# Kernel tuning notes

Hardware: AMD Instinct MI355X
Metric: run time of the kernel (lower is better)

The kernel has to match this reference:

```python
import jax, jax.numpy as jnp
import numpy as np

D = 1024
H = 16
HD = D // H
N_TEXT = 256
N_VISION = 256
N_FRAMES = 12


def setup_inputs() -> dict:
    key = jax.random.key(0)
    ks = jax.random.split(key, 10)
    s = 1.0 / np.sqrt(D)
    return {
        "text_hidden_states": jax.random.normal(ks[0], (N_TEXT, D), jnp.float32),
        "vision_hidden_states": jax.random.normal(ks[1], (N_VISION, N_FRAMES, D), jnp.float32),
        "wq": jax.random.normal(ks[2], (D, D), jnp.float32) * s,
        "bq": jnp.zeros((D,), jnp.float32),
        "wk": jax.random.normal(ks[3], (D, D), jnp.float32) * s,
        "bk": jnp.zeros((D,), jnp.float32),
        "wv": jax.random.normal(ks[4], (D, D), jnp.float32) * s,
        "bv": jnp.zeros((D,), jnp.float32),
        "wo": jax.random.normal(ks[5], (D, D), jnp.float32) * s,
        "bo": jnp.zeros((D,), jnp.float32),
    }


def reference(text_hidden_states, vision_hidden_states, wq, bq, wk, bk, wv, bv, wo, bo):
    n_text = text_hidden_states.shape[0]
    n_vision, n_frames, _ = vision_hidden_states.shape
    # projections (torch Linear: x @ W.T + b)
    q = (text_hidden_states @ wq.T + bq).reshape(n_text, H, HD)            # [t,h,d]
    k = (vision_hidden_states @ wk.T + bk).reshape(n_vision, n_frames, H, HD)  # [v,f,h,d]
    v = (vision_hidden_states @ wv.T + bv).reshape(n_vision, n_frames, H, HD)  # [v,f,h,d]
    # shared query broadcast over vision batch: scores [v,h,f,t]
    scores = jnp.einsum("vfhd,thd->vhft", k, q) / jnp.sqrt(jnp.asarray(HD, scores_dtype := q.dtype))
    probs = jax.nn.softmax(scores, axis=2)  # softmax over frames (dim=2)
    # attn_output [v,t,h,d] -> [v,t,D]
    out = jnp.einsum("vfhd,vhft->vthd", v, probs).reshape(n_vision, n_text, D)
    return out @ wo.T + bo
```

## Files before the change

### kernel.cpp

```cpp
#include <hip/hip_runtime.h>

typedef short bf16x8 __attribute__((ext_vector_type(8)));
typedef float f32x4 __attribute__((ext_vector_type(4)));

__device__ __forceinline__ unsigned short f2bf(float f) {
  union { float f; unsigned u; } x; x.f = f;
  unsigned u = x.u;
  u += 0x7fffu + ((u >> 16) & 1u);
  return (unsigned short)(u >> 16);
}

__global__ __launch_bounds__(256) void cvt_all(
    const float* __restrict__ text, const float* __restrict__ vis,
    const float* __restrict__ wq, const float* __restrict__ wk,
    const float* __restrict__ wv, const float* __restrict__ wo,
    unsigned short* __restrict__ o0, unsigned short* __restrict__ o1,
    unsigned short* __restrict__ o2, unsigned short* __restrict__ o3,
    unsigned short* __restrict__ o4, unsigned short* __restrict__ o5)
{
  long i4 = (long)blockIdx.x * 256 + threadIdx.x;
  const float* src; unsigned short* dst; long base;
  if      (i4 <   65536) { src = text; dst = o0; base = 0; }
  else if (i4 <  851968) { src = vis;  dst = o1; base = 65536; }
  else if (i4 < 1114112) { src = wq;   dst = o2; base = 851968; }
  else if (i4 < 1376256) { src = wk;   dst = o3; base = 1114112; }
  else if (i4 < 1638400) { src = wv;   dst = o4; base = 1376256; }
  else                   { src = wo;   dst = o5; base = 1638400; }
  long li = i4 - base;
  float4 f = reinterpret_cast<const float4*>(src)[li];
  uint2 u;
  u.x = (unsigned)f2bf(f.x) | ((unsigned)f2bf(f.y) << 16);
  u.y = (unsigned)f2bf(f.z) | ((unsigned)f2bf(f.w) << 16);
  reinterpret_cast<uint2*>(dst)[li] = u;
}

__global__ __launch_bounds__(256) void gemm_abt_bf16(
    const unsigned short* __restrict__ A,
    const unsigned short* __restrict__ B,
    unsigned short* __restrict__ C,
    const float* __restrict__ bias,
    int K, int lda, int ldb, int ldc)
{
  __shared__ unsigned short As[64][40];
  __shared__ unsigned short Bs[64][40];
  const int m0 = blockIdx.y * 64, n0 = blockIdx.x * 64;
  const int tid = threadIdx.x;
  const int lane = tid & 63, w = tid >> 6;
  const int wm = w >> 1, wn = w & 1;
  const int r16 = lane & 15, kg = lane >> 4;
  const int srow = tid >> 2, sseg = tid & 3;

  const f32x4 fzero = {0.f, 0.f, 0.f, 0.f};
  f32x4 acc[2][2];
#pragma unroll
  for (int i = 0; i < 2; ++i)
#pragma unroll
    for (int j = 0; j < 2; ++j) acc[i][j] = fzero;

  for (int k0 = 0; k0 < K; k0 += 32) {
    __syncthreads();
    *reinterpret_cast<int4*>(&As[srow][sseg * 8]) =
        *reinterpret_cast<const int4*>(&A[(long)(m0 + srow) * lda + k0 + sseg * 8]);
    *reinterpret_cast<int4*>(&Bs[srow][sseg * 8]) =
        *reinterpret_cast<const int4*>(&B[(long)(n0 + srow) * ldb + k0 + sseg * 8]);
    __syncthreads();
    bf16x8 a[2], b[2];
#pragma unroll
    for (int i = 0; i < 2; ++i)
      a[i] = *reinterpret_cast<const bf16x8*>(&As[wm * 32 + i * 16 + r16][kg * 8]);
#pragma unroll
    for (int j = 0; j < 2; ++j)
      b[j] = *reinterpret_cast<const bf16x8*>(&Bs[wn * 32 + j * 16 + r16][kg * 8]);
#pragma unroll
    for (int i = 0; i < 2; ++i)
#pragma unroll
      for (int j = 0; j < 2; ++j)
        acc[i][j] = __builtin_amdgcn_mfma_f32_16x16x32_bf16(a[i], b[j], acc[i][j], 0, 0, 0);
  }
#pragma unroll
  for (int i = 0; i < 2; ++i) {
#pragma unroll
    for (int j = 0; j < 2; ++j) {
      const int row = m0 + wm * 32 + i * 16 + kg * 4;
      const int col = n0 + wn * 32 + j * 16 + r16;
      const float bv = bias ? bias[col] : 0.f;
#pragma unroll
      for (int r = 0; r < 4; ++r)
        C[(long)(row + r) * ldc + col] = f2bf(acc[i][j][r] + bv);
    }
  }
}

__global__ __launch_bounds__(256) void scores_softmax(
    const unsigned short* __restrict__ Kp,
    const unsigned short* __restrict__ Qp,
    unsigned short* __restrict__ P)
{
  const int h = blockIdx.x, v = blockIdx.y;
  const int tid = threadIdx.x, lane = tid & 63, w = tid >> 6;
  const int r16 = lane & 15, kg = lane >> 4;
  __shared__ unsigned short Ks[16][72];
  __shared__ unsigned short Qs[256][72];

  if (tid < 96) {
    const int f = tid >> 3, seg = tid & 7;
    *reinterpret_cast<int4*>(&Ks[f][seg * 8]) =
        *reinterpret_cast<const int4*>(&Kp[(long)(v * 12 + f) * 1024 + h * 64 + seg * 8]);
  } else if (tid < 128) {
    const int f = 12 + ((tid - 96) >> 3), seg = (tid - 96) & 7;
    int4 z; z.x = z.y = z.z = z.w = 0;
    *reinterpret_cast<int4*>(&Ks[f][seg * 8]) = z;
  }
#pragma unroll
  for (int rep = 0; rep < 8; ++rep) {
    const int row = rep * 32 + (tid >> 3), seg = tid & 7;
    *reinterpret_cast<int4*>(&Qs[row][seg * 8]) =
        *reinterpret_cast<const int4*>(&Qp[(long)row * 1024 + h * 64 + seg * 8]);
  }
  __syncthreads();

  const f32x4 fzero = {0.f, 0.f, 0.f, 0.f};
  f32x4 acc[4];
#pragma unroll
  for (int j = 0; j < 4; ++j) acc[j] = fzero;

#pragma unroll
  for (int kk = 0; kk < 64; kk += 32) {
    bf16x8 a = *reinterpret_cast<const bf16x8*>(&Ks[r16][kk + kg * 8]);
#pragma unroll
    for (int j = 0; j < 4; ++j) {
      bf16x8 b = *reinterpret_cast<const bf16x8*>(&Qs[w * 64 + j * 16 + r16][kk + kg * 8]);
      acc[j] = __builtin_amdgcn_mfma_f32_16x16x32_bf16(a, b, acc[j], 0, 0, 0);
    }
  }
#pragma unroll
  for (int j = 0; j < 4; ++j) {
    float lm = -1e30f;
    if (kg < 3) {
#pragma unroll
      for (int r = 0; r < 4; ++r) lm = fmaxf(lm, acc[j][r] * 0.125f);
    }
    lm = fmaxf(lm, __shfl_xor(lm, 16));
    lm = fmaxf(lm, __shfl_xor(lm, 32));
    float p[4]; float ls = 0.f;
    if (kg < 3) {
#pragma unroll
      for (int r = 0; r < 4; ++r) { p[r] = __expf(acc[j][r] * 0.125f - lm); ls += p[r]; }
    }
    ls += __shfl_xor(ls, 16);
    ls += __shfl_xor(ls, 32);
    const float inv = 1.f / ls;
    if (kg < 3) {
      const int t = w * 64 + j * 16 + r16;
#pragma unroll
      for (int r = 0; r < 4; ++r)
        P[((long)v * 256 + t) * 192 + (kg * 4 + r) * 16 + h] = f2bf(p[r] * inv);
    }
  }
}

__global__ __launch_bounds__(256) void combine(
    const unsigned short* __restrict__ VPp,
    const unsigned short* __restrict__ Wo,
    const unsigned short* __restrict__ P,
    const float* __restrict__ bo,
    float* __restrict__ out)
{
  const int wgid = blockIdx.x;
  const int xcd = wgid & 7, idx = wgid >> 3;
  const int v = ((idx & 31) << 3) | xcd;
  const int n0 = (idx >> 5) << 6;

  const int tid = threadIdx.x, lane = tid & 63, w = tid >> 6;
  const int r16 = lane & 15, kg = lane >> 4;

  __shared__ unsigned short BsAll[64 * 192];
  __shared__ unsigned short VPs[2][16 * 64];
  __shared__ unsigned short Wos[2][64 * 64];

  for (int it = 0; it < 8; ++it) {
    const int hbase = it * 2;
    __syncthreads();
    {
      const int hh = tid >> 7, row = (tid >> 3) & 15, slot = tid & 7;
      int4 val;
      if (row < 12)
        val = *reinterpret_cast<const int4*>(
            &VPp[(long)(v * 12 + row) * 1024 + (hbase + hh) * 64 + slot * 8]);
      else { val.x = 0; val.y = 0; val.z = 0; val.w = 0; }
      *reinterpret_cast<int4*>(&VPs[hh][row * 64 + ((slot ^ (row & 7)) << 3)]) = val;
    }
    {
      const int hh = tid >> 7;
      const int row = (tid & 127) >> 1, slot0 = (tid & 1) * 4;
#pragma unroll
      for (int rep = 0; rep < 4; ++rep) {
        const int slot = slot0 + rep;
        *reinterpret_cast<int4*>(&Wos[hh][row * 64 + ((slot ^ (row & 7)) << 3)]) =
            *reinterpret_cast<const int4*>(
                &Wo[(long)(n0 + row) * 1024 + (hbase + hh) * 64 + slot * 8]);
      }
    }
    __syncthreads();
    const int hh = w >> 1, oh = w & 1, h = hbase + hh;
    f32x4 accp[2] = {{0.f,0.f,0.f,0.f},{0.f,0.f,0.f,0.f}};
#pragma unroll
    for (int kk = 0; kk < 64; kk += 32) {
      const int slot = (kk >> 3) + kg;
      bf16x8 a = *reinterpret_cast<const bf16x8*>(
          &VPs[hh][r16 * 64 + ((slot ^ (r16 & 7)) << 3)]);
#pragma unroll
      for (int j = 0; j < 2; ++j) {
        const int orow = oh * 32 + j * 16 + r16;
        bf16x8 b = *reinterpret_cast<const bf16x8*>(
            &Wos[hh][orow * 64 + ((slot ^ (orow & 7)) << 3)]);
        accp[j] = __builtin_amdgcn_mfma_f32_16x16x32_bf16(a, b, accp[j], 0, 0, 0);
      }
    }
#pragma unroll
    for (int j = 0; j < 2; ++j) {
#pragma unroll
      for (int r = 0; r < 4; ++r) {
        const int f = kg * 4 + r;
        if (f < 12) {
          const int o = oh * 32 + j * 16 + r16;
          const int k = f * 16 + h;
          BsAll[o * 192 + (((k >> 3) ^ (o & 7)) << 3) + (k & 7)] = f2bf(accp[j][r]);
        }
      }
    }
  }
  __syncthreads();

  const f32x4 fzero = {0.f, 0.f, 0.f, 0.f};
  f32x4 acc[4][4];
#pragma unroll
  for (int i = 0; i < 4; ++i)
#pragma unroll
    for (int j = 0; j < 4; ++j) acc[i][j] = fzero;

  const unsigned short* Pv = P + (long)v * 256 * 192;
#pragma unroll
  for (int k0 = 0; k0 < 192; k0 += 32) {
    bf16x8 b[4];
#pragma unroll
    for (int j = 0; j < 4; ++j) {
      const int row = j * 16 + r16;
      const int slot = (k0 >> 3) + kg;
      b[j] = *reinterpret_cast<const bf16x8*>(
          &BsAll[row * 192 + ((slot ^ (row & 7)) << 3)]);
    }
#pragma unroll
    for (int i = 0; i < 4; ++i) {
      bf16x8 a = *reinterpret_cast<const bf16x8*>(
          &Pv[(long)(w * 64 + i * 16 + r16) * 192 + k0 + kg * 8]);
#pragma unroll
      for (int j = 0; j < 4; ++j)
        acc[i][j] = __builtin_amdgcn_mfma_f32_16x16x32_bf16(a, b[j], acc[i][j], 0, 0, 0);
    }
  }
#pragma unroll
  for (int i = 0; i < 4; ++i) {
#pragma unroll
    for (int j = 0; j < 4; ++j) {
      const int trow = w * 64 + i * 16 + kg * 4;
      const int col = n0 + j * 16 + r16;
      const float bv = bo[col];
#pragma unroll
      for (int r = 0; r < 4; ++r)
        out[((long)v * 256 + trow + r) * 1024 + col] = acc[i][j][r] + bv;
    }
  }
}

extern "C" void kernel_launch(void* const* d_in, const int* in_sizes, int n_in,
                              void* d_out, int out_size, void* d_ws, size_t ws_size,
                              hipStream_t stream) {
  const float* text = (const float*)d_in[0];
  const float* vis  = (const float*)d_in[1];
  const float* wq   = (const float*)d_in[2];
  const float* bq   = (const float*)d_in[3];
  const float* wk   = (const float*)d_in[4];
  const float* bk   = (const float*)d_in[5];
  const float* wv   = (const float*)d_in[6];
  const float* bv   = (const float*)d_in[7];
  const float* wo   = (const float*)d_in[8];
  const float* bo   = (const float*)d_in[9];
  float* out = (float*)d_out;

  unsigned short* text16 = (unsigned short*)d_ws;
  unsigned short* vis16  = text16 + 262144;
  unsigned short* wq16   = vis16  + 3145728;
  unsigned short* wk16   = wq16   + 1048576;
  unsigned short* wv16   = wk16   + 1048576;
  unsigned short* wo16   = wv16   + 1048576;
  unsigned short* q16    = wo16   + 1048576;
  unsigned short* k16    = q16    + 262144;
  unsigned short* vp16   = k16    + 3145728;
  unsigned short* P      = vp16   + 3145728;

  cvt_all<<<7424, 256, 0, stream>>>(text, vis, wq, wk, wv, wo,
                                    text16, vis16, wq16, wk16, wv16, wo16);
  gemm_abt_bf16<<<dim3(16, 4), 256, 0, stream>>>(text16, wq16, q16, bq, 1024, 1024, 1024, 1024);
  gemm_abt_bf16<<<dim3(16, 48), 256, 0, stream>>>(vis16, wk16, k16, bk, 1024, 1024, 1024, 1024);
  gemm_abt_bf16<<<dim3(16, 48), 256, 0, stream>>>(vis16, wv16, vp16, bv, 1024, 1024, 1024, 1024);
  scores_softmax<<<dim3(16, 256), 256, 0, stream>>>(k16, q16, P);
  combine<<<4096, 256, 0, stream>>>(vp16, wo16, P, bo, out);
}
```

Before: 279.1 us.

## Merge K/V projection launches and load combine operands directly from global memory

The separate K and V projection GEMMs become one launch, with grid z choosing between the two weight/output pairs, which saves a kernel launch and fills the device better. In the combine kernel, the per-head VP·Wo stage no longer stages VP and Wo through shared memory with barriers. Each wave now handles four heads and reads its MFMA fragments straight from global memory. The P operand loads are also software-prefetched one k-step ahead. Together these remove eight barrier pairs per block, at the cost of more uncoalesced global and L2 traffic for Wo fragments and higher register pressure.

After: 273.3 us. 1.02x faster.

```diff
diff --git a/kernel.cpp b/kernel.cpp
--- a/kernel.cpp
+++ b/kernel.cpp
@@ -91,6 +91,70 @@
   }
 }
 
+__global__ __launch_bounds__(256) void gemm_abt_bf16_kv(
+    const unsigned short* __restrict__ A,
+    const unsigned short* __restrict__ B0,
+    const unsigned short* __restrict__ B1,
+    unsigned short* __restrict__ C0,
+    unsigned short* __restrict__ C1,
+    const float* __restrict__ bias0,
+    const float* __restrict__ bias1,
+    int K, int lda, int ldb, int ldc)
+{
+  const unsigned short* B = blockIdx.z ? B1 : B0;
+  unsigned short* C = blockIdx.z ? C1 : C0;
+  const float* bias = blockIdx.z ? bias1 : bias0;
+
+  __shared__ unsigned short As[64][40];
+  __shared__ unsigned short Bs[64][40];
+  const int m0 = blockIdx.y * 64, n0 = blockIdx.x * 64;
+  const int tid = threadIdx.x;
+  const int lane = tid & 63, w = tid >> 6;
+  const int wm = w >> 1, wn = w & 1;
+  const int r16 = lane & 15, kg = lane >> 4;
+  const int srow = tid >> 2, sseg = tid & 3;
+
+  const f32x4 fzero = {0.f, 0.f, 0.f, 0.f};
+  f32x4 acc[2][2];
+#pragma unroll
+  for (int i = 0; i < 2; ++i)
+#pragma unroll
+    for (int j = 0; j < 2; ++j) acc[i][j] = fzero;
+
+  for (int k0 = 0; k0 < K; k0 += 32) {
+    __syncthreads();
+    *reinterpret_cast<int4*>(&As[srow][sseg * 8]) =
+        *reinterpret_cast<const int4*>(&A[(long)(m0 + srow) * lda + k0 + sseg * 8]);
+    *reinterpret_cast<int4*>(&Bs[srow][sseg * 8]) =
+        *reinterpret_cast<const int4*>(&B[(long)(n0 + srow) * ldb + k0 + sseg * 8]);
+    __syncthreads();
+    bf16x8 a[2], b[2];
+#pragma unroll
+    for (int i = 0; i < 2; ++i)
+      a[i] = *reinterpret_cast<const bf16x8*>(&As[wm * 32 + i * 16 + r16][kg * 8]);
+#pragma unroll
+    for (int j = 0; j < 2; ++j)
+      b[j] = *reinterpret_cast<const bf16x8*>(&Bs[wn * 32 + j * 16 + r16][kg * 8]);
+#pragma unroll
+    for (int i = 0; i < 2; ++i)
+#pragma unroll
+      for (int j = 0; j < 2; ++j)
+        acc[i][j] = __builtin_amdgcn_mfma_f32_16x16x32_bf16(a[i], b[j], acc[i][j], 0, 0, 0);
+  }
+#pragma unroll
+  for (int i = 0; i < 2; ++i) {
+#pragma unroll
+    for (int j = 0; j < 2; ++j) {
+      const int row = m0 + wm * 32 + i * 16 + kg * 4;
+      const int col = n0 + wn * 32 + j * 16 + r16;
+      const float bv = bias ? bias[col] : 0.f;
+#pragma unroll
+      for (int r = 0; r < 4; ++r)
+        C[(long)(row + r) * ldc + col] = f2bf(acc[i][j][r] + bv);
+    }
+  }
+}
+
 __global__ __launch_bounds__(256) void scores_softmax(
     const unsigned short* __restrict__ Kp,
     const unsigned short* __restrict__ Qp,
@@ -108,7 +172,7 @@
         *reinterpret_cast<const int4*>(&Kp[(long)(v * 12 + f) * 1024 + h * 64 + seg * 8]);
   } else if (tid < 128) {
     const int f = 12 + ((tid - 96) >> 3), seg = (tid - 96) & 7;
-    int4 z; z.x = z.y = z.z = z.w = 0;
+    int4 z; z.x = 0; z.y = 0; z.z = 0; z.w = 0;
     *reinterpret_cast<int4*>(&Ks[f][seg * 8]) = z;
   }
 #pragma unroll
@@ -175,73 +239,67 @@
   const int r16 = lane & 15, kg = lane >> 4;
 
   __shared__ unsigned short BsAll[64 * 192];
-  __shared__ unsigned short VPs[2][16 * 64];
-  __shared__ unsigned short Wos[2][64 * 64];
-
-  for (int it = 0; it < 8; ++it) {
-    const int hbase = it * 2;
-    __syncthreads();
-    {
-      const int hh = tid >> 7, row = (tid >> 3) & 15, slot = tid & 7;
-      int4 val;
-      if (row < 12)
-        val = *reinterpret_cast<const int4*>(
-            &VPp[(long)(v * 12 + row) * 1024 + (hbase + hh) * 64 + slot * 8]);
-      else { val.x = 0; val.y = 0; val.z = 0; val.w = 0; }
-      *reinterpret_cast<int4*>(&VPs[hh][row * 64 + ((slot ^ (row & 7)) << 3)]) = val;
-    }
-    {
-      const int hh = tid >> 7;
-      const int row = (tid & 127) >> 1, slot0 = (tid & 1) * 4;
-#pragma unroll
-      for (int rep = 0; rep < 4; ++rep) {
-        const int slot = slot0 + rep;
-        *reinterpret_cast<int4*>(&Wos[hh][row * 64 + ((slot ^ (row & 7)) << 3)]) =
-            *reinterpret_cast<const int4*>(
-                &Wo[(long)(n0 + row) * 1024 + (hbase + hh) * 64 + slot * 8]);
-      }
-    }
-    __syncthreads();
-    const int hh = w >> 1, oh = w & 1, h = hbase + hh;
-    f32x4 accp[2] = {{0.f,0.f,0.f,0.f},{0.f,0.f,0.f,0.f}};
+
+  const unsigned short* VPv = VPp + (long)v * 12 * 1024;
+#pragma unroll
+  for (int hi = 0; hi < 4; ++hi) {
+    const int h = (w << 2) + hi;
+    const int db = h * 64;
+    f32x4 accp[4] = {{0.f,0.f,0.f,0.f},{0.f,0.f,0.f,0.f},{0.f,0.f,0.f,0.f},{0.f,0.f,0.f,0.f}};
 #pragma unroll
     for (int kk = 0; kk < 64; kk += 32) {
-      const int slot = (kk >> 3) + kg;
-      bf16x8 a = *reinterpret_cast<const bf16x8*>(
-          &VPs[hh][r16 * 64 + ((slot ^ (r16 & 7)) << 3)]);
-#pragma unroll
-      for (int j = 0; j < 2; ++j) {
-        const int orow = oh * 32 + j * 16 + r16;
-        bf16x8 b = *reinterpret_cast<const bf16x8*>(
-            &Wos[hh][orow * 64 + ((slot ^ (orow & 7)) << 3)]);
-        accp[j] = __builtin_amdgcn_mfma_f32_16x16x32_bf16(a, b, accp[j], 0, 0, 0);
-      }
-    }
-#pragma unroll
-    for (int j = 0; j < 2; ++j) {
+      bf16x8 a = {0,0,0,0,0,0,0,0};
+      if (r16 < 12)
+        a = *reinterpret_cast<const bf16x8*>(&VPv[(long)r16 * 1024 + db + kk + kg * 8]);
+      bf16x8 bfr[4];
+#pragma unroll
+      for (int j = 0; j < 4; ++j)
+        bfr[j] = *reinterpret_cast<const bf16x8*>(
+            &Wo[(long)(n0 + j * 16 + r16) * 1024 + db + kk + kg * 8]);
+#pragma unroll
+      for (int j = 0; j < 4; ++j)
+        accp[j] = __builtin_amdgcn_mfma_f32_16x16x32_bf16(a, bfr[j], accp[j], 0, 0, 0);
+    }
+#pragma unroll
+    for (int j = 0; j < 4; ++j) {
 #pragma unroll
       for (int r = 0; r < 4; ++r) {
         const int f = kg * 4 + r;
         if (f < 12) {
-          const int o = oh * 32 + j * 16 + r16;
+          const int o = j * 16 + r16;
           const int k = f * 16 + h;
           BsAll[o * 192 + (((k >> 3) ^ (o & 7)) << 3) + (k & 7)] = f2bf(accp[j][r]);
         }
       }
     }
   }
+
+  const unsigned short* Pv = P + (long)v * 256 * 192;
+  bf16x8 aP[4];
+#pragma unroll
+  for (int i = 0; i < 4; ++i)
+    aP[i] = *reinterpret_cast<const bf16x8*>(
+        &Pv[(long)(w * 64 + i * 16 + r16) * 192 + kg * 8]);
+
   __syncthreads();
 
-  const f32x4 fzero = {0.f, 0.f, 0.f, 0.f};
   f32x4 acc[4][4];
 #pragma unroll
   for (int i = 0; i < 4; ++i)
 #pragma unroll
-    for (int j = 0; j < 4; ++j) acc[i][j] = fzero;
-
-  const unsigned short* Pv = P + (long)v * 256 * 192;
+    for (int j = 0; j < 4; ++j) { f32x4 z = {0.f,0.f,0.f,0.f}; acc[i][j] = z; }
+
 #pragma unroll
   for (int k0 = 0; k0 < 192; k0 += 32) {
+    bf16x8 aC[4];
+#pragma unroll
+    for (int i = 0; i < 4; ++i) aC[i] = aP[i];
+    if (k0 < 160) {
+#pragma unroll
+      for (int i = 0; i < 4; ++i)
+        aP[i] = *reinterpret_cast<const bf16x8*>(
+            &Pv[(long)(w * 64 + i * 16 + r16) * 192 + (k0 + 32) + kg * 8]);
+    }
     bf16x8 b[4];
 #pragma unroll
     for (int j = 0; j < 4; ++j) {
@@ -251,13 +309,10 @@
           &BsAll[row * 192 + ((slot ^ (row & 7)) << 3)]);
     }
 #pragma unroll
-    for (int i = 0; i < 4; ++i) {
-      bf16x8 a = *reinterpret_cast<const bf16x8*>(
-          &Pv[(long)(w * 64 + i * 16 + r16) * 192 + k0 + kg * 8]);
+    for (int i = 0; i < 4; ++i)
 #pragma unroll
       for (int j = 0; j < 4; ++j)
-        acc[i][j] = __builtin_amdgcn_mfma_f32_16x16x32_bf16(a, b[j], acc[i][j], 0, 0, 0);
-    }
+        acc[i][j] = __builtin_amdgcn_mfma_f32_16x16x32_bf16(aC[i], b[j], acc[i][j], 0, 0, 0);
   }
 #pragma unroll
   for (int i = 0; i < 4; ++i) {
@@ -302,8 +357,8 @@
   cvt_all<<<7424, 256, 0, stream>>>(text, vis, wq, wk, wv, wo,
                                     text16, vis16, wq16, wk16, wv16, wo16);
   gemm_abt_bf16<<<dim3(16, 4), 256, 0, stream>>>(text16, wq16, q16, bq, 1024, 1024, 1024, 1024);
-  gemm_abt_bf16<<<dim3(16, 48), 256, 0, stream>>>(vis16, wk16, k16, bk, 1024, 1024, 1024, 1024);
-  gemm_abt_bf16<<<dim3(16, 48), 256, 0, stream>>>(vis16, wv16, vp16, bv, 1024, 1024, 1024, 1024);
+  gemm_abt_bf16_kv<<<dim3(16, 48, 2), 256, 0, stream>>>(
+      vis16, wk16, wv16, k16, vp16, bk, bv, 1024, 1024, 1024, 1024);
   scores_softmax<<<dim3(16, 256), 256, 0, stream>>>(k16, q16, P);
   combine<<<4096, 256, 0, stream>>>(vp16, wo16, P, bo, out);
 }
```
